# Kernel tuning notes

Hardware: AMD Instinct MI355X
Metric: run time of the kernel (lower is better)

The kernel has to match this reference:

```python
import jax, jax.numpy as jnp
import numpy as np

K = 3
EPS = 1e-08
N_SRC = 65536   # source points
M_QRY = 262144  # query points
C_FEAT = 128


def setup_inputs() -> dict:
    key = jax.random.key(0)
    k1, k2, k3, k4 = jax.random.split(key, 4)
    s_feats = jax.random.normal(k1, (N_SRC, C_FEAT), dtype=jnp.float32)
    q_points = jax.random.normal(k2, (M_QRY, 3), dtype=jnp.float32)
    s_points = jax.random.normal(k3, (N_SRC, 3), dtype=jnp.float32)
    neighbor_indices = jax.random.randint(k4, (M_QRY, K), 0, N_SRC, dtype=jnp.int64)
    return {
        "s_feats": s_feats,
        "q_points": q_points,
        "s_points": s_points,
        "neighbor_indices": neighbor_indices,
    }


def reference(s_feats, q_points, s_points, neighbor_indices):
    # k-NN inverse-distance interpolation (k > 1 branch of KNNInterpolate)
    knn_idx = neighbor_indices[:, :K]            # [M, k]
    knn_points = s_points[knn_idx]               # [M, k, 3] gather
    knn_feats = s_feats[knn_idx]                 # [M, k, C] gather
    # squared distances query -> each neighbor
    d2 = jnp.sum((q_points[:, None, :] - knn_points) ** 2, axis=-1)  # [M, k]
    w = 1.0 / (d2 + EPS)                          # inverse-distance weights
    w = w / jnp.sum(w, axis=-1, keepdims=True)    # normalize over k
    q_feats = jnp.einsum("mk,mkc->mc", w, knn_feats)  # weighted reduction
    return q_feats
```

## Files before the change

kernel.cpp:

```cpp
#include <hip/hip_runtime.h>

#define KNN_K 3
#define KNN_EPS 1e-8f
#define C_FEAT 128
#define M_QRY 262144

__global__ __launch_bounds__(256) void knn_interp_kernel(
    const float* __restrict__ s_feats,
    const float* __restrict__ q_points,
    const float* __restrict__ s_points,
    const int*   __restrict__ nbr_idx,
    float* __restrict__ out)
{
    const int t  = blockIdx.x * blockDim.x + threadIdx.x;
    const int m  = t >> 5;
    const int c4 = t & 31;
    if (m >= M_QRY) return;

    const int i0 = nbr_idx[m * 3 + 0];
    const int i1 = nbr_idx[m * 3 + 1];
    const int i2 = nbr_idx[m * 3 + 2];

    const float qx = q_points[m * 3 + 0];
    const float qy = q_points[m * 3 + 1];
    const float qz = q_points[m * 3 + 2];

    float dx, dy, dz;
    dx = qx - s_points[i0 * 3 + 0];
    dy = qy - s_points[i0 * 3 + 1];
    dz = qz - s_points[i0 * 3 + 2];
    float w0 = 1.0f / (dx * dx + dy * dy + dz * dz + KNN_EPS);

    dx = qx - s_points[i1 * 3 + 0];
    dy = qy - s_points[i1 * 3 + 1];
    dz = qz - s_points[i1 * 3 + 2];
    float w1 = 1.0f / (dx * dx + dy * dy + dz * dz + KNN_EPS);

    dx = qx - s_points[i2 * 3 + 0];
    dy = qy - s_points[i2 * 3 + 1];
    dz = qz - s_points[i2 * 3 + 2];
    float w2 = 1.0f / (dx * dx + dy * dy + dz * dz + KNN_EPS);

    const float inv_sum = 1.0f / (w0 + w1 + w2);
    w0 *= inv_sum; w1 *= inv_sum; w2 *= inv_sum;

    const float4* __restrict__ f0 = (const float4*)(s_feats + (size_t)i0 * C_FEAT);
    const float4* __restrict__ f1 = (const float4*)(s_feats + (size_t)i1 * C_FEAT);
    const float4* __restrict__ f2 = (const float4*)(s_feats + (size_t)i2 * C_FEAT);

    const float4 a = f0[c4];
    const float4 b = f1[c4];
    const float4 c = f2[c4];

    float4 r;
    r.x = w0 * a.x + w1 * b.x + w2 * c.x;
    r.y = w0 * a.y + w1 * b.y + w2 * c.y;
    r.z = w0 * a.z + w1 * b.z + w2 * c.z;
    r.w = w0 * a.w + w1 * b.w + w2 * c.w;

    ((float4*)(out + (size_t)m * C_FEAT))[c4] = r;
}

extern "C" void kernel_launch(void* const* d_in, const int* in_sizes, int n_in,
                              void* d_out, int out_size, void* d_ws, size_t ws_size,
                              hipStream_t stream) {
    const float* s_feats  = (const float*)d_in[0];
    const float* q_points = (const float*)d_in[1];
    const float* s_points = (const float*)d_in[2];
    const int*   nbr_idx  = (const int*)d_in[3];
    float* out = (float*)d_out;

    const int total_threads = M_QRY * 32;
    const int block = 256;
    const int grid  = (total_threads + block - 1) / block;

    knn_interp_kernel<<<grid, block, 0, stream>>>(s_feats, q_points, s_points,
                                                  nbr_idx, out);
}
```

Baseline: 207.3 us.

## Process two queries per thread, issue gathers early, use nontemporal stores

```diff
diff --git a/kernel.cpp b/kernel.cpp
--- a/kernel.cpp
+++ b/kernel.cpp
@@ -1,9 +1,11 @@
 #include <hip/hip_runtime.h>
 
-#define KNN_K 3
 #define KNN_EPS 1e-8f
 #define C_FEAT 128
 #define M_QRY 262144
+#define QPT 2
+
+typedef float f4 __attribute__((ext_vector_type(4)));
 
 __global__ __launch_bounds__(256) void knn_interp_kernel(
     const float* __restrict__ s_feats,
@@ -13,52 +15,70 @@
     float* __restrict__ out)
 {
     const int t  = blockIdx.x * blockDim.x + threadIdx.x;
-    const int m  = t >> 5;
+    const int g  = t >> 5;
     const int c4 = t & 31;
-    if (m >= M_QRY) return;
+    const int m0 = g * QPT;
+    const int m1 = m0 + 1;
 
-    const int i0 = nbr_idx[m * 3 + 0];
-    const int i1 = nbr_idx[m * 3 + 1];
-    const int i2 = nbr_idx[m * 3 + 2];
+    const int a0 = nbr_idx[m0 * 3 + 0];
+    const int a1 = nbr_idx[m0 * 3 + 1];
+    const int a2 = nbr_idx[m0 * 3 + 2];
+    const int b0 = nbr_idx[m1 * 3 + 0];
+    const int b1 = nbr_idx[m1 * 3 + 1];
+    const int b2 = nbr_idx[m1 * 3 + 2];
 
-    const float qx = q_points[m * 3 + 0];
-    const float qy = q_points[m * 3 + 1];
-    const float qz = q_points[m * 3 + 2];
+    const f4 va0 = ((const f4*)(s_feats + (size_t)a0 * C_FEAT))[c4];
+    const f4 va1 = ((const f4*)(s_feats + (size_t)a1 * C_FEAT))[c4];
+    const f4 va2 = ((const f4*)(s_feats + (size_t)a2 * C_FEAT))[c4];
+    const f4 vb0 = ((const f4*)(s_feats + (size_t)b0 * C_FEAT))[c4];
+    const f4 vb1 = ((const f4*)(s_feats + (size_t)b1 * C_FEAT))[c4];
+    const f4 vb2 = ((const f4*)(s_feats + (size_t)b2 * C_FEAT))[c4];
+
+    const float qax = q_points[m0 * 3 + 0];
+    const float qay = q_points[m0 * 3 + 1];
+    const float qaz = q_points[m0 * 3 + 2];
+    const float qbx = q_points[m1 * 3 + 0];
+    const float qby = q_points[m1 * 3 + 1];
+    const float qbz = q_points[m1 * 3 + 2];
 
     float dx, dy, dz;
-    dx = qx - s_points[i0 * 3 + 0];
-    dy = qy - s_points[i0 * 3 + 1];
-    dz = qz - s_points[i0 * 3 + 2];
-    float w0 = 1.0f / (dx * dx + dy * dy + dz * dz + KNN_EPS);
 
-    dx = qx - s_points[i1 * 3 + 0];
-    dy = qy - s_points[i1 * 3 + 1];
-    dz = qz - s_points[i1 * 3 + 2];
-    float w1 = 1.0f / (dx * dx + dy * dy + dz * dz + KNN_EPS);
+    dx = qax - s_points[a0 * 3 + 0];
+    dy = qay - s_points[a0 * 3 + 1];
+    dz = qaz - s_points[a0 * 3 + 2];
+    float wa0 = __builtin_amdgcn_rcpf(dx * dx + dy * dy + dz * dz + KNN_EPS);
+    dx = qax - s_points[a1 * 3 + 0];
+    dy = qay - s_points[a1 * 3 + 1];
+    dz = qaz - s_points[a1 * 3 + 2];
+    float wa1 = __builtin_amdgcn_rcpf(dx * dx + dy * dy + dz * dz + KNN_EPS);
+    dx = qax - s_points[a2 * 3 + 0];
+    dy = qay - s_points[a2 * 3 + 1];
+    dz = qaz - s_points[a2 * 3 + 2];
+    float wa2 = __builtin_amdgcn_rcpf(dx * dx + dy * dy + dz * dz + KNN_EPS);
 
-    dx = qx - s_points[i2 * 3 + 0];
-    dy = qy - s_points[i2 * 3 + 1];
-    dz = qz - s_points[i2 * 3 + 2];
-    float w2 = 1.0f / (dx * dx + dy * dy + dz * dz + KNN_EPS);
+    dx = qbx - s_points[b0 * 3 + 0];
+    dy = qby - s_points[b0 * 3 + 1];
+    dz = qbz - s_points[b0 * 3 + 2];
+    float wb0 = __builtin_amdgcn_rcpf(dx * dx + dy * dy + dz * dz + KNN_EPS);
+    dx = qbx - s_points[b1 * 3 + 0];
+    dy = qby - s_points[b1 * 3 + 1];
+    dz = qbz - s_points[b1 * 3 + 2];
+    float wb1 = __builtin_amdgcn_rcpf(dx * dx + dy * dy + dz * dz + KNN_EPS);
+    dx = qbx - s_points[b2 * 3 + 0];
+    dy = qby - s_points[b2 * 3 + 1];
+    dz = qbz - s_points[b2 * 3 + 2];
+    float wb2 = __builtin_amdgcn_rcpf(dx * dx + dy * dy + dz * dz + KNN_EPS);
 
-    const float inv_sum = 1.0f / (w0 + w1 + w2);
-    w0 *= inv_sum; w1 *= inv_sum; w2 *= inv_sum;
+    const float inv_a = __builtin_amdgcn_rcpf(wa0 + wa1 + wa2);
+    const float inv_b = __builtin_amdgcn_rcpf(wb0 + wb1 + wb2);
+    const float na0 = wa0 * inv_a, na1 = wa1 * inv_a, na2 = wa2 * inv_a;
+    const float nb0 = wb0 * inv_b, nb1 = wb1 * inv_b, nb2 = wb2 * inv_b;
 
-    const float4* __restrict__ f0 = (const float4*)(s_feats + (size_t)i0 * C_FEAT);
-    const float4* __restrict__ f1 = (const float4*)(s_feats + (size_t)i1 * C_FEAT);
-    const float4* __restrict__ f2 = (const float4*)(s_feats + (size_t)i2 * C_FEAT);
+    const f4 ra = na0 * va0 + na1 * va1 + na2 * va2;
+    const f4 rb = nb0 * vb0 + nb1 * vb1 + nb2 * vb2;
 
-    const float4 a = f0[c4];
-    const float4 b = f1[c4];
-    const float4 c = f2[c4];
-
-    float4 r;
-    r.x = w0 * a.x + w1 * b.x + w2 * c.x;
-    r.y = w0 * a.y + w1 * b.y + w2 * c.y;
-    r.z = w0 * a.z + w1 * b.z + w2 * c.z;
-    r.w = w0 * a.w + w1 * b.w + w2 * c.w;
-
-    ((float4*)(out + (size_t)m * C_FEAT))[c4] = r;
+    __builtin_nontemporal_store(ra, (f4*)(out + (size_t)m0 * C_FEAT) + c4);
+    __builtin_nontemporal_store(rb, (f4*)(out + (size_t)m1 * C_FEAT) + c4);
 }
 
 extern "C" void kernel_launch(void* const* d_in, const int* in_sizes, int n_in,
@@ -70,7 +90,7 @@
     const int*   nbr_idx  = (const int*)d_in[3];
     float* out = (float*)d_out;
 
-    const int total_threads = M_QRY * 32;
+    const int total_threads = M_QRY * 32 / QPT;
     const int block = 256;
     const int grid  = (total_threads + block - 1) / block;
 
```

New measurement: 208.1 us. No clear change (+0.4%).

## Process four queries per 32-lane group with batched gathers, fast rcp, nontemporal stores

Applied to the files above, without the earlier changes.

```diff
diff --git a/kernel.cpp b/kernel.cpp
--- a/kernel.cpp
+++ b/kernel.cpp
@@ -1,9 +1,11 @@
 #include <hip/hip_runtime.h>
 
-#define KNN_K 3
 #define KNN_EPS 1e-8f
 #define C_FEAT 128
 #define M_QRY 262144
+#define QPT 4
+
+typedef float f4 __attribute__((ext_vector_type(4)));
 
 __global__ __launch_bounds__(256) void knn_interp_kernel(
     const float* __restrict__ s_feats,
@@ -13,52 +15,51 @@
     float* __restrict__ out)
 {
     const int t  = blockIdx.x * blockDim.x + threadIdx.x;
-    const int m  = t >> 5;
+    const int g  = t >> 5;
     const int c4 = t & 31;
-    if (m >= M_QRY) return;
+    const int mbase = g * QPT;
 
-    const int i0 = nbr_idx[m * 3 + 0];
-    const int i1 = nbr_idx[m * 3 + 1];
-    const int i2 = nbr_idx[m * 3 + 2];
+    int idx[QPT][3];
+#pragma unroll
+    for (int q = 0; q < QPT; ++q) {
+#pragma unroll
+        for (int k = 0; k < 3; ++k)
+            idx[q][k] = nbr_idx[(mbase + q) * 3 + k];
+    }
 
-    const float qx = q_points[m * 3 + 0];
-    const float qy = q_points[m * 3 + 1];
-    const float qz = q_points[m * 3 + 2];
+    f4 v[QPT][3];
+#pragma unroll
+    for (int q = 0; q < QPT; ++q) {
+#pragma unroll
+        for (int k = 0; k < 3; ++k)
+            v[q][k] = ((const f4*)(s_feats + (size_t)idx[q][k] * C_FEAT))[c4];
+    }
 
-    float dx, dy, dz;
-    dx = qx - s_points[i0 * 3 + 0];
-    dy = qy - s_points[i0 * 3 + 1];
-    dz = qz - s_points[i0 * 3 + 2];
-    float w0 = 1.0f / (dx * dx + dy * dy + dz * dz + KNN_EPS);
+    float w[QPT][3];
+#pragma unroll
+    for (int q = 0; q < QPT; ++q) {
+        const int m = mbase + q;
+        const float qx = q_points[m * 3 + 0];
+        const float qy = q_points[m * 3 + 1];
+        const float qz = q_points[m * 3 + 2];
+#pragma unroll
+        for (int k = 0; k < 3; ++k) {
+            const int s = idx[q][k];
+            const float dx = qx - s_points[s * 3 + 0];
+            const float dy = qy - s_points[s * 3 + 1];
+            const float dz = qz - s_points[s * 3 + 2];
+            w[q][k] = __builtin_amdgcn_rcpf(dx * dx + dy * dy + dz * dz + KNN_EPS);
+        }
+    }
 
-    dx = qx - s_points[i1 * 3 + 0];
-    dy = qy - s_points[i1 * 3 + 1];
-    dz = qz - s_points[i1 * 3 + 2];
-    float w1 = 1.0f / (dx * dx + dy * dy + dz * dz + KNN_EPS);
-
-    dx = qx - s_points[i2 * 3 + 0];
-    dy = qy - s_points[i2 * 3 + 1];
-    dz = qz - s_points[i2 * 3 + 2];
-    float w2 = 1.0f / (dx * dx + dy * dy + dz * dz + KNN_EPS);
-
-    const float inv_sum = 1.0f / (w0 + w1 + w2);
-    w0 *= inv_sum; w1 *= inv_sum; w2 *= inv_sum;
-
-    const float4* __restrict__ f0 = (const float4*)(s_feats + (size_t)i0 * C_FEAT);
-    const float4* __restrict__ f1 = (const float4*)(s_feats + (size_t)i1 * C_FEAT);
-    const float4* __restrict__ f2 = (const float4*)(s_feats + (size_t)i2 * C_FEAT);
-
-    const float4 a = f0[c4];
-    const float4 b = f1[c4];
-    const float4 c = f2[c4];
-
-    float4 r;
-    r.x = w0 * a.x + w1 * b.x + w2 * c.x;
-    r.y = w0 * a.y + w1 * b.y + w2 * c.y;
-    r.z = w0 * a.z + w1 * b.z + w2 * c.z;
-    r.w = w0 * a.w + w1 * b.w + w2 * c.w;
-
-    ((float4*)(out + (size_t)m * C_FEAT))[c4] = r;
+#pragma unroll
+    for (int q = 0; q < QPT; ++q) {
+        const float inv = __builtin_amdgcn_rcpf(w[q][0] + w[q][1] + w[q][2]);
+        const f4 r = (w[q][0] * inv) * v[q][0]
+                   + (w[q][1] * inv) * v[q][1]
+                   + (w[q][2] * inv) * v[q][2];
+        __builtin_nontemporal_store(r, (f4*)(out + (size_t)(mbase + q) * C_FEAT) + c4);
+    }
 }
 
 extern "C" void kernel_launch(void* const* d_in, const int* in_sizes, int n_in,
@@ -70,7 +71,7 @@
     const int*   nbr_idx  = (const int*)d_in[3];
     float* out = (float*)d_out;
 
-    const int total_threads = M_QRY * 32;
+    const int total_threads = M_QRY * 32 / QPT;
     const int block = 256;
     const int grid  = (total_threads + block - 1) / block;
 
```

After: 208.4 us. Within noise of the previous version (+0.5%).
